# Performance work log

Hardware: AMD Instinct MI355X
Metric: run time of the kernel (lower is better)

## Reference

```python
import jax, jax.numpy as jnp
import numpy as np

B, I, H = 16384, 512, 512


def setup_inputs() -> dict:
    key = jax.random.key(0)
    ks = jax.random.split(key, 14)
    s_in = 1.0 / np.sqrt(I)
    s_h = 1.0 / np.sqrt(H)
    inp = {
        "z": jax.random.normal(ks[0], (B, H), jnp.float32),
        "x": jax.random.normal(ks[1], (B, I), jnp.float32),
        # input->hidden weights (torch Linear stores [out, in])
        "W_i": jax.random.uniform(ks[2], (H, I), jnp.float32, -s_in, s_in),
        "W_f": jax.random.uniform(ks[3], (H, I), jnp.float32, -s_in, s_in),
        "W_c": jax.random.uniform(ks[4], (H, I), jnp.float32, -s_in, s_in),
        "W_o": jax.random.uniform(ks[5], (H, I), jnp.float32, -s_in, s_in),
        "b_i": jax.random.uniform(ks[6], (H,), jnp.float32, -s_in, s_in),
        "b_f": jax.random.uniform(ks[7], (H,), jnp.float32, -s_in, s_in),
        "b_c": jax.random.uniform(ks[8], (H,), jnp.float32, -s_in, s_in),
        "b_o": jax.random.uniform(ks[9], (H,), jnp.float32, -s_in, s_in),
        # hidden->hidden weights (no bias)
        "U_i": jax.random.uniform(ks[10], (H, H), jnp.float32, -s_h, s_h),
        "U_f": jax.random.uniform(ks[11], (H, H), jnp.float32, -s_h, s_h),
        "U_c": jax.random.uniform(ks[12], (H, H), jnp.float32, -s_h, s_h),
        "U_o": jax.random.uniform(ks[13], (H, H), jnp.float32, -s_h, s_h),
    }
    return inp


def reference(z, x, W_i, W_f, W_c, W_o, b_i, b_f, b_c, b_o, U_i, U_f, U_c, U_o):
    # Fuse the 4 input GEMMs and 4 hidden GEMMs into two batched matmuls.
    Wx = jnp.stack([W_i, W_f, W_c, W_o])            # [4, H, I]
    bx = jnp.stack([b_i, b_f, b_c, b_o])            # [4, H]
    Uz = jnp.stack([U_i, U_f, U_c, U_o])            # [4, H, H]
    gx = jnp.einsum('bi,ghi->gbh', x, Wx) + bx[:, None, :]   # [4, B, H]
    gz = jnp.einsum('bh,gkh->gbk', z, Uz)                     # [4, B, H]
    pre = gx + gz
    i = jax.nn.sigmoid(pre[0])
    f = jax.nn.sigmoid(pre[1])
    g = jnp.tanh(pre[2])
    o = jax.nn.sigmoid(pre[3])
    c_next = f * z + i * g
    h_next = o * jnp.tanh(c_next)
    # u=None, tau=None path: z_next = h_next
    return (h_next, c_next)
```

## Files before the change

### kernel.cpp

```cpp
#include <hip/hip_runtime.h>
#include <hip/hip_bf16.h>
#include <stdint.h>

#define B_DIM 16384
#define H_DIM 512
#define KTOT  1024
#define NP    2048

typedef __attribute__((ext_vector_type(4))) float floatx4;
typedef __attribute__((ext_vector_type(4))) int   int4v;

#define SCALE_X 6.0f
#define S_IN    0.04419417382415922f
#define QA      (127.0f / SCALE_X)
#define QB      (127.0f / S_IN)
#define DQ      ((SCALE_X / 127.0f) * (S_IN / 127.0f))

static __device__ __forceinline__ unsigned int q4(const float* s, float sc) {
  unsigned int w = 0;
#pragma unroll
  for (int i = 0; i < 4; ++i) {
    int q = __float2int_rn(fminf(fmaxf(s[i] * sc, -127.f), 127.f));
    w |= ((unsigned int)(q & 255)) << (8 * i);
  }
  return w;
}

static __device__ __forceinline__ int4v quant16(const float* src, float sc) {
  float buf[16];
#pragma unroll
  for (int i = 0; i < 4; ++i)
    *reinterpret_cast<floatx4*>(buf + 4 * i) =
        *reinterpret_cast<const floatx4*>(src + 4 * i);
  int4v o;
#pragma unroll
  for (int i = 0; i < 4; ++i) o[i] = (int)q4(buf + 4 * i, sc);
  return o;
}

__global__ __launch_bounds__(256) void pack_kernel(
    const float* __restrict__ x, const float* __restrict__ z,
    const float* __restrict__ Wi, const float* __restrict__ Wf,
    const float* __restrict__ Wc, const float* __restrict__ Wo,
    const float* __restrict__ Ui, const float* __restrict__ Uf,
    const float* __restrict__ Uc, const float* __restrict__ Uo,
    int* __restrict__ Ap, int* __restrict__ Bp) {
  int b = blockIdx.x;
  if (b < 4096) {
    int u    = b * 256 + threadIdx.x;
    int lane = u & 63;
    int m4   = (u >> 6) & 3;
    int mh   = (u >> 8) & 1;
    int wr   = (u >> 9) & 1;
    int kt   = (u >> 10) & 15;
    int bm   = u >> 14;
    int row  = bm * 256 + wr * 128 + mh * 64 + m4 * 16 + (lane & 15);
    int k    = kt * 64 + ((lane >> 4) << 4);
    const float* src = (k < 512) ? (x + (uint64_t)row * 512 + k)
                                 : (z + (uint64_t)row * 512 + (k - 512));
    *reinterpret_cast<int4v*>(Ap + (uint64_t)u * 4) = quant16(src, QA);
  } else {
    int u    = (b - 4096) * 256 + threadIdx.x;
    int lane = u & 63;
    int g    = (u >> 6) & 3;
    int wc   = (u >> 8) & 1;
    int kt   = (u >> 9) & 15;
    int bn   = u >> 13;
    int h    = bn * 32 + wc * 16 + (lane & 15);
    int k    = kt * 64 + ((lane >> 4) << 4);
    const float* src;
    if (k < 512) {
      const float* W = (g == 0) ? Wi : (g == 1) ? Wf : (g == 2) ? Wc : Wo;
      src = W + (uint64_t)h * 512 + k;
    } else {
      const float* U = (g == 0) ? Ui : (g == 1) ? Uf : (g == 2) ? Uc : Uo;
      src = U + (uint64_t)h * 512 + (k - 512);
    }
    *reinterpret_cast<int4v*>(Bp + (uint64_t)u * 4) = quant16(src, QB);
  }
}

#define LOADSET(AS, BS, PA, PB)                                             \
  _Pragma("unroll")                                                         \
  for (int g = 0; g < 4; ++g)                                               \
    BS[g] = *reinterpret_cast<const int4v*>((PB) + g * 256);                \
  _Pragma("unroll")                                                         \
  for (int m = 0; m < 8; ++m)                                               \
    AS[m] = *reinterpret_cast<const int4v*>(                                \
        (PA) + (m >> 2) * 1024 + (m & 3) * 256);

#define COMPUTE(AS, BS)                                                     \
  __builtin_amdgcn_s_setprio(1);                                            \
  _Pragma("unroll")                                                         \
  for (int m = 0; m < 8; ++m)                                               \
    _Pragma("unroll")                                                       \
    for (int g = 0; g < 4; ++g)                                             \
      acc[m][g] = __builtin_amdgcn_mfma_i32_16x16x64_i8(                    \
          AS[m], BS[g], acc[m][g], 0, 0, 0);                                \
  __builtin_amdgcn_s_setprio(0);

__global__ __launch_bounds__(256, 2) void lstm_gemm_kernel(
    const int* __restrict__ Ap, const int* __restrict__ Bp,
    const float* __restrict__ z,
    const float* __restrict__ b_i, const float* __restrict__ b_f,
    const float* __restrict__ b_c, const float* __restrict__ b_o,
    float* __restrict__ out) {
  int tid  = threadIdx.x;
  int bid  = blockIdx.x;
  int sw   = (bid & 7) * 128 + (bid >> 3);
  int bn   = sw & 15;
  int bm   = sw >> 4;
  int lane = tid & 63;
  int wid  = tid >> 6;
  int wr   = wid >> 1;
  int wc   = wid & 1;

  int4v acc[8][4];
#pragma unroll
  for (int m = 0; m < 8; ++m)
#pragma unroll
    for (int g = 0; g < 4; ++g)
      acc[m][g] = (int4v){0, 0, 0, 0};

  const int* pA = Ap + (uint64_t)bm * (16 * 4096) + wr * 2048 + lane * 4;
  const int* pB = Bp + (uint64_t)bn * (16 * 2048) + wc * 1024 + lane * 4;

  int4v a0[8], b0[4], a1[8], b1[4];

  LOADSET(a0, b0, pA, pB)
  LOADSET(a1, b1, pA + 4096, pB + 2048)

#pragma unroll 1
  for (int kt = 0; kt < 14; kt += 2) {
    const int* pA2 = pA + (kt + 2) * 4096;
    const int* pB2 = pB + (kt + 2) * 2048;
    COMPUTE(a0, b0)
    LOADSET(a0, b0, pA2, pB2)
    COMPUTE(a1, b1)
    LOADSET(a1, b1, pA2 + 4096, pB2 + 2048)
  }
  COMPUTE(a0, b0)
  COMPUTE(a1, b1)

  int h = bn * 32 + wc * 16 + (lane & 15);
  float vbi = b_i[h], vbf = b_f[h], vbc = b_c[h], vbo = b_o[h];
  int rbase = bm * 256 + wr * 128 + ((lane >> 4) << 2);
  float* outH = out;
  float* outC = out + (uint64_t)B_DIM * H_DIM;
#pragma unroll
  for (int m = 0; m < 8; ++m) {
#pragma unroll
    for (int j = 0; j < 4; ++j) {
      int r = rbase + m * 16 + j;
      float pi = (float)acc[m][0][j] * DQ + vbi;
      float pf = (float)acc[m][1][j] * DQ + vbf;
      float pc = (float)acc[m][2][j] * DQ + vbc;
      float po = (float)acc[m][3][j] * DQ + vbo;
      float gi = 1.f / (1.f + __expf(-pi));
      float gf = 1.f / (1.f + __expf(-pf));
      float gc = 1.f - 2.f / (__expf(2.f * pc) + 1.f);
      float go = 1.f / (1.f + __expf(-po));
      float zv = z[(uint64_t)r * H_DIM + h];
      float cn = gf * zv + gi * gc;
      float hn = go * (1.f - 2.f / (__expf(2.f * cn) + 1.f));
      outH[(uint64_t)r * H_DIM + h] = hn;
      outC[(uint64_t)r * H_DIM + h] = cn;
    }
  }
}

extern "C" void kernel_launch(void* const* d_in, const int* in_sizes, int n_in,
                              void* d_out, int out_size, void* d_ws, size_t ws_size,
                              hipStream_t stream) {
  const float* z  = (const float*)d_in[0];
  const float* x  = (const float*)d_in[1];
  const float* Wi = (const float*)d_in[2];
  const float* Wf = (const float*)d_in[3];
  const float* Wc = (const float*)d_in[4];
  const float* Wo = (const float*)d_in[5];
  const float* bi = (const float*)d_in[6];
  const float* bf = (const float*)d_in[7];
  const float* bc = (const float*)d_in[8];
  const float* bo = (const float*)d_in[9];
  const float* Ui = (const float*)d_in[10];
  const float* Uf = (const float*)d_in[11];
  const float* Uc = (const float*)d_in[12];
  const float* Uo = (const float*)d_in[13];

  int* Ap = (int*)d_ws;
  int* Bp = (int*)((char*)d_ws + (size_t)B_DIM * KTOT);
  float* out = (float*)d_out;

  hipLaunchKernelGGL(pack_kernel, dim3(4608), dim3(256), 0, stream,
                     x, z, Wi, Wf, Wc, Wo, Ui, Uf, Uc, Uo, Ap, Bp);
  hipLaunchKernelGGL(lstm_gemm_kernel, dim3(1024), dim3(256), 0, stream,
                     Ap, Bp, z, bi, bf, bc, bo, out);
}
```

Before: 74.46 us.

## Stage full-K B tile in LDS and shrink block tile to 256x16x4 gates

```diff
diff --git a/kernel.cpp b/kernel.cpp
--- a/kernel.cpp
+++ b/kernel.cpp
@@ -63,10 +63,9 @@
     int u    = (b - 4096) * 256 + threadIdx.x;
     int lane = u & 63;
     int g    = (u >> 6) & 3;
-    int wc   = (u >> 8) & 1;
-    int kt   = (u >> 9) & 15;
-    int bn   = u >> 13;
-    int h    = bn * 32 + wc * 16 + (lane & 15);
+    int kt   = (u >> 8) & 15;
+    int bn   = u >> 12;
+    int h    = bn * 16 + (lane & 15);
     int k    = kt * 64 + ((lane >> 4) << 4);
     const float* src;
     if (k < 512) {
@@ -80,24 +79,27 @@
   }
 }
 
-#define LOADSET(AS, BS, PA, PB)                                             \
+#define LOADA(AS, PA)                                                       \
   _Pragma("unroll")                                                         \
-  for (int g = 0; g < 4; ++g)                                               \
-    BS[g] = *reinterpret_cast<const int4v*>((PB) + g * 256);                \
-  _Pragma("unroll")                                                         \
-  for (int m = 0; m < 8; ++m)                                               \
-    AS[m] = *reinterpret_cast<const int4v*>(                                \
-        (PA) + (m >> 2) * 1024 + (m & 3) * 256);
-
-#define COMPUTE(AS, BS)                                                     \
-  __builtin_amdgcn_s_setprio(1);                                            \
-  _Pragma("unroll")                                                         \
-  for (int m = 0; m < 8; ++m)                                               \
+  for (int m = 0; m < 4; ++m)                                               \
+    AS[m] = *reinterpret_cast<const int4v*>((PA) + m * 256);
+
+#define COMPUTE(AS, KT)                                                     \
+  {                                                                         \
+    int4v bF[4];                                                            \
     _Pragma("unroll")                                                       \
     for (int g = 0; g < 4; ++g)                                             \
-      acc[m][g] = __builtin_amdgcn_mfma_i32_16x16x64_i8(                    \
-          AS[m], BS[g], acc[m][g], 0, 0, 0);                                \
-  __builtin_amdgcn_s_setprio(0);
+      bF[g] = *reinterpret_cast<const int4v*>(                              \
+          bLds + (KT) * 1024 + g * 256 + lane * 4);                         \
+    __builtin_amdgcn_s_setprio(1);                                          \
+    _Pragma("unroll")                                                       \
+    for (int m = 0; m < 4; ++m)                                             \
+      _Pragma("unroll")                                                     \
+      for (int g = 0; g < 4; ++g)                                           \
+        acc[m][g] = __builtin_amdgcn_mfma_i32_16x16x64_i8(                  \
+            AS[m], bF[g], acc[m][g], 0, 0, 0);                              \
+    __builtin_amdgcn_s_setprio(0);                                          \
+  }
 
 __global__ __launch_bounds__(256, 2) void lstm_gemm_kernel(
     const int* __restrict__ Ap, const int* __restrict__ Bp,
@@ -105,50 +107,59 @@
     const float* __restrict__ b_i, const float* __restrict__ b_f,
     const float* __restrict__ b_c, const float* __restrict__ b_o,
     float* __restrict__ out) {
+  __shared__ int bLds[16384];
+
   int tid  = threadIdx.x;
   int bid  = blockIdx.x;
-  int sw   = (bid & 7) * 128 + (bid >> 3);
-  int bn   = sw & 15;
-  int bm   = sw >> 4;
+  int sw   = (bid & 7) * 256 + (bid >> 3);
+  int bn   = sw & 31;
+  int bm   = sw >> 5;
   int lane = tid & 63;
-  int wid  = tid >> 6;
-  int wr   = wid >> 1;
-  int wc   = wid & 1;
-
-  int4v acc[8][4];
-#pragma unroll
-  for (int m = 0; m < 8; ++m)
+  int w    = tid >> 6;
+
+  const int* gB = Bp + (uint64_t)bn * 16384;
+#pragma unroll
+  for (int r = 0; r < 16; ++r)
+    __builtin_amdgcn_global_load_lds(
+        (const __attribute__((address_space(1))) void*)(gB + r * 1024 + tid * 4),
+        (__attribute__((address_space(3))) void*)(bLds + r * 1024 + tid * 4),
+        16, 0, 0);
+
+  const int* pA = Ap + (uint64_t)bm * (16 * 4096)
+                  + (w >> 1) * 2048 + (w & 1) * 1024 + lane * 4;
+
+  int4v a0[4], a1[4];
+  LOADA(a0, pA)
+  LOADA(a1, pA + 4096)
+
+  asm volatile("s_waitcnt vmcnt(8)" ::: "memory");
+  __builtin_amdgcn_s_barrier();
+
+  int4v acc[4][4];
+#pragma unroll
+  for (int m = 0; m < 4; ++m)
 #pragma unroll
     for (int g = 0; g < 4; ++g)
       acc[m][g] = (int4v){0, 0, 0, 0};
-
-  const int* pA = Ap + (uint64_t)bm * (16 * 4096) + wr * 2048 + lane * 4;
-  const int* pB = Bp + (uint64_t)bn * (16 * 2048) + wc * 1024 + lane * 4;
-
-  int4v a0[8], b0[4], a1[8], b1[4];
-
-  LOADSET(a0, b0, pA, pB)
-  LOADSET(a1, b1, pA + 4096, pB + 2048)
 
 #pragma unroll 1
   for (int kt = 0; kt < 14; kt += 2) {
     const int* pA2 = pA + (kt + 2) * 4096;
-    const int* pB2 = pB + (kt + 2) * 2048;
-    COMPUTE(a0, b0)
-    LOADSET(a0, b0, pA2, pB2)
-    COMPUTE(a1, b1)
-    LOADSET(a1, b1, pA2 + 4096, pB2 + 2048)
-  }
-  COMPUTE(a0, b0)
-  COMPUTE(a1, b1)
-
-  int h = bn * 32 + wc * 16 + (lane & 15);
+    COMPUTE(a0, kt)
+    LOADA(a0, pA2)
+    COMPUTE(a1, kt + 1)
+    LOADA(a1, pA2 + 4096)
+  }
+  COMPUTE(a0, 14)
+  COMPUTE(a1, 15)
+
+  int h = bn * 16 + (lane & 15);
   float vbi = b_i[h], vbf = b_f[h], vbc = b_c[h], vbo = b_o[h];
-  int rbase = bm * 256 + wr * 128 + ((lane >> 4) << 2);
+  int rbase = bm * 256 + w * 64 + ((lane >> 4) << 2);
   float* outH = out;
   float* outC = out + (uint64_t)B_DIM * H_DIM;
 #pragma unroll
-  for (int m = 0; m < 8; ++m) {
+  for (int m = 0; m < 4; ++m) {
 #pragma unroll
     for (int j = 0; j < 4; ++j) {
       int r = rbase + m * 16 + j;
@@ -193,6 +204,6 @@
 
   hipLaunchKernelGGL(pack_kernel, dim3(4608), dim3(256), 0, stream,
                      x, z, Wi, Wf, Wc, Wo, Ui, Uf, Uc, Uo, Ap, Bp);
-  hipLaunchKernelGGL(lstm_gemm_kernel, dim3(1024), dim3(256), 0, stream,
+  hipLaunchKernelGGL(lstm_gemm_kernel, dim3(2048), dim3(256), 0, stream,
                      Ap, Bp, z, bi, bf, bc, bo, out);
 }
```

Measured after the change: 78.42 us. +5.3%, slower.
